# Optimization experiments

Measured on AMD Instinct MI355X. Metric: run time of the kernel, lower is better.

Reference implementation:

```python
import jax, jax.numpy as jnp
import numpy as np

B, T, D, H, F = 4, 2048, 512, 8, 2048
WINDOW = 128
HD = D // H
EPS = 1e-5


def layer_norm(x, g, b):
    mu = jnp.mean(x, axis=-1, keepdims=True)
    var = jnp.mean(jnp.square(x - mu), axis=-1, keepdims=True)
    return (x - mu) * jax.lax.rsqrt(var + EPS) * g + b


def setup_inputs() -> dict:
    key = jax.random.key(0)
    ks = jax.random.split(key, 5)
    s = 0.02
    return {
        "x": jax.random.normal(ks[0], (B, T, D), dtype=jnp.float32),
        "in_proj_w": jax.random.normal(ks[1], (3 * D, D), dtype=jnp.float32) * s,
        "in_proj_b": jnp.zeros((3 * D,), dtype=jnp.float32),
        "out_w": jax.random.normal(ks[2], (D, D), dtype=jnp.float32) * s,
        "out_b": jnp.zeros((D,), dtype=jnp.float32),
        "ln1_g": jnp.ones((D,), dtype=jnp.float32),
        "ln1_b": jnp.zeros((D,), dtype=jnp.float32),
        "ln2_g": jnp.ones((D,), dtype=jnp.float32),
        "ln2_b": jnp.zeros((D,), dtype=jnp.float32),
        "w1": jax.random.normal(ks[3], (F, D), dtype=jnp.float32) * s,
        "b1": jnp.zeros((F,), dtype=jnp.float32),
        "w2": jax.random.normal(ks[4], (D, F), dtype=jnp.float32) * s,
        "b2": jnp.zeros((D,), dtype=jnp.float32),
    }


def reference(x, in_proj_w, in_proj_b, out_w, out_b, ln1_g, ln1_b, ln2_g, ln2_b, w1, b1, w2, b2):
    # pre-norm sliding-window causal self-attention
    x2 = layer_norm(x, ln1_g, ln1_b)
    qkv = x2 @ in_proj_w.T + in_proj_b  # (B,T,3D)
    q, k, v = jnp.split(qkv, 3, axis=-1)
    q = q.reshape(B, T, H, HD)
    k = k.reshape(B, T, H, HD)
    v = v.reshape(B, T, H, HD)
    scale = 1.0 / np.sqrt(HD).astype(np.float32)
    scores = jnp.einsum("bthd,bshd->bhts", q, k) * scale  # dense (B,H,T,T)
    idx = jnp.arange(T)
    i = idx[:, None]
    j = idx[None, :]
    allowed = (j <= i) & (j >= i - WINDOW + 1)  # (T,T) bool, True = attend
    scores = jnp.where(allowed[None, None], scores, -jnp.inf)
    attn = jax.nn.softmax(scores, axis=-1)
    ctx = jnp.einsum("bhts,bshd->bthd", attn, v).reshape(B, T, D)
    attn_out = ctx @ out_w.T + out_b
    x = x + attn_out  # dropout is identity in eval
    # FFN block
    x3 = layer_norm(x, ln2_g, ln2_b)
    h = jax.nn.gelu(x3 @ w1.T + b1, approximate=False)
    x = x + h @ w2.T + b2
    return x
```

## Files before the change

### kernel.cpp

```cpp
#include <hip/hip_runtime.h>
#include <math.h>

constexpr int Bn = 4;
constexpr int Tn = 2048;
constexpr int Dn = 512;
constexpr int Hn = 8;
constexpr int HDn = 64;
constexpr int Fn = 2048;
constexpr int WIN = 128;
constexpr float EPS = 1e-5f;
constexpr int Mrows = Bn * Tn;
constexpr int QKVD = 3 * Dn;

using short8 = __attribute__((ext_vector_type(8))) short;
using f32x4  = __attribute__((ext_vector_type(4))) float;

__device__ __forceinline__ short f2bf(float f) {
    unsigned u = __float_as_uint(f);
    unsigned r = (u + 0x7FFFu + ((u >> 16) & 1u)) >> 16;
    return (short)r;
}

__device__ __forceinline__ float gelu_exact(float v) {
    return 0.5f * v * (1.0f + erff(v * 0.70710678118654752f));
}

__device__ __forceinline__ void async16(const short* g, short* l) {
    __builtin_amdgcn_global_load_lds(
        (const __attribute__((address_space(1))) void*)g,
        (__attribute__((address_space(3))) void*)l,
        16, 0, 0);
}

__global__ __launch_bounds__(256) void cvt_bf16(const float* __restrict__ src,
                                                short* __restrict__ dst, int n4)
{
    int i = blockIdx.x * 256 + threadIdx.x;
    if (i < n4) {
        float4 v = ((const float4*)src)[i];
        short4 o;
        o.x = f2bf(v.x); o.y = f2bf(v.y); o.z = f2bf(v.z); o.w = f2bf(v.w);
        ((short4*)dst)[i] = o;
    }
}

__global__ __launch_bounds__(64) void ln_kernel(const float* __restrict__ x,
                                                const float* __restrict__ g,
                                                const float* __restrict__ b,
                                                short* __restrict__ y)
{
    int row = blockIdx.x;
    int lane = threadIdx.x;
    const float4* xr = (const float4*)(x + (size_t)row * Dn);
    float4 v0 = xr[lane];
    float4 v1 = xr[lane + 64];
    float s = v0.x + v0.y + v0.z + v0.w + v1.x + v1.y + v1.z + v1.w;
#pragma unroll
    for (int off = 32; off >= 1; off >>= 1) s += __shfl_xor(s, off, 64);
    float mu = s * (1.0f / Dn);
    float d0x = v0.x - mu, d0y = v0.y - mu, d0z = v0.z - mu, d0w = v0.w - mu;
    float d1x = v1.x - mu, d1y = v1.y - mu, d1z = v1.z - mu, d1w = v1.w - mu;
    float q = d0x*d0x + d0y*d0y + d0z*d0z + d0w*d0w
            + d1x*d1x + d1y*d1y + d1z*d1z + d1w*d1w;
#pragma unroll
    for (int off = 32; off >= 1; off >>= 1) q += __shfl_xor(q, off, 64);
    float inv = rsqrtf(q * (1.0f / Dn) + EPS);
    const float4* gr = (const float4*)g;
    const float4* br = (const float4*)b;
    float4 g0 = gr[lane], g1 = gr[lane + 64];
    float4 b0 = br[lane], b1 = br[lane + 64];
    short4 a0, a1;
    a0.x = f2bf(d0x * inv * g0.x + b0.x);
    a0.y = f2bf(d0y * inv * g0.y + b0.y);
    a0.z = f2bf(d0z * inv * g0.z + b0.z);
    a0.w = f2bf(d0w * inv * g0.w + b0.w);
    a1.x = f2bf(d1x * inv * g1.x + b1.x);
    a1.y = f2bf(d1y * inv * g1.y + b1.y);
    a1.z = f2bf(d1z * inv * g1.z + b1.z);
    a1.w = f2bf(d1w * inv * g1.w + b1.w);
    short4* yr = (short4*)(y + (size_t)row * Dn);
    yr[lane] = a0;
    yr[lane + 64] = a1;
}

template <int MODE, int BK>
__global__ __launch_bounds__(256) void gemm_mfma(const short* __restrict__ A,
                                                 const short* __restrict__ Bw,
                                                 const float* __restrict__ bias,
                                                 const float* __restrict__ resid,
                                                 void* __restrict__ Cout,
                                                 short* __restrict__ q_out,
                                                 short* __restrict__ k_out,
                                                 short* __restrict__ v_out,
                                                 int M, int N, int K)
{
    constexpr int NCH = BK / 8;
    constexpr int LGN = (BK == 32) ? 2 : 3;
    constexpr int RPI = 512 / BK;
    constexpr int NI  = 32 / RPI;
    constexpr int BUF = 128 * BK;
    constexpr int KK  = BK / 32;
    constexpr int SMSZ = (4 * BUF > 17408) ? 4 * BUF : 17408;
    __shared__ short SMEM[SMSZ];
    short* Asb = SMEM;
    short* Bsb = SMEM + 2 * BUF;

    int tid = threadIdx.x;
    int w = tid >> 6, lane = tid & 63;
    int wr = w >> 1, wc = w & 1;
    int m0 = blockIdx.y * 128, n0 = blockIdx.x * 128;
    int quad = lane >> 4, l16 = lane & 15;

    f32x4 zero = {0.f, 0.f, 0.f, 0.f};
    f32x4 acc[4][4];
#pragma unroll
    for (int i = 0; i < 4; ++i)
#pragma unroll
        for (int j = 0; j < 4; ++j) acc[i][j] = zero;

    int rl = lane >> LGN;
    int ch = lane & (NCH - 1);
    const short* Ag[NI];
    const short* Bg[NI];
    int ldsOff[NI];
#pragma unroll
    for (int s = 0; s < NI; ++s) {
        int rowl = w * 32 + s * RPI + rl;
        int csw = (ch ^ ((rowl * BK >> 6) & (NCH - 1))) * 8;
        Ag[s] = A + (size_t)(m0 + rowl) * K + csw;
        Bg[s] = Bw + (size_t)(n0 + rowl) * K + csw;
        ldsOff[s] = (w * 32 + s * RPI) * BK;
    }

    auto stage = [&](int kt, int pp) {
#pragma unroll
        for (int s = 0; s < NI; ++s) {
            async16(Ag[s] + kt, Asb + pp * BUF + ldsOff[s]);
            async16(Bg[s] + kt, Bsb + pp * BUF + ldsOff[s]);
        }
    };

    stage(0, 0);
    int p = 0;
    for (int kt = 0; kt < K; kt += BK) {
        __syncthreads();
        if (kt + BK < K) stage(kt + BK, p ^ 1);
        short8 aF[KK][4], bF[KK][4];
#pragma unroll
        for (int kk = 0; kk < KK; ++kk)
#pragma unroll
            for (int i = 0; i < 4; ++i) {
                int ra = wr * 64 + i * 16 + l16;
                int rb = wc * 64 + i * 16 + l16;
                int cs = ((kk * 4 + quad) ^ ((ra * BK >> 6) & (NCH - 1))) * 8;
                aF[kk][i] = *(const short8*)(Asb + p * BUF + ra * BK + cs);
                bF[kk][i] = *(const short8*)(Bsb + p * BUF + rb * BK + cs);
            }
#pragma unroll
        for (int kk = 0; kk < KK; ++kk)
#pragma unroll
            for (int i = 0; i < 4; ++i)
#pragma unroll
                for (int j = 0; j < 4; ++j)
                    acc[i][j] = __builtin_amdgcn_mfma_f32_16x16x32_bf16(
                        aF[kk][i], bF[kk][j], acc[i][j], 0, 0, 0);
        p ^= 1;
    }

    if constexpr (MODE == 3) {
        __syncthreads();
        short* rp = SMEM + w * 4352;
        int b = m0 >> 11;
        int ncol0 = n0 + wc * 64;
        int sec = ncol0 >> 9;
        int h = (ncol0 & 511) >> 6;
        int bh = b * 8 + h;
        int t0 = (m0 & 2047) + wr * 64;
        if (sec == 2) {
#pragma unroll
            for (int j = 0; j < 4; ++j) {
                int d = j * 16 + l16;
                float bv = bias[ncol0 + j * 16 + l16];
#pragma unroll
                for (int i = 0; i < 4; ++i)
#pragma unroll
                    for (int r = 0; r < 4; ++r)
                        rp[d * 68 + i * 16 + quad * 4 + r] = f2bf(acc[i][j][r] + bv);
            }
#pragma unroll
            for (int it = 0; it < 8; ++it) {
                int row = it * 8 + (lane >> 3);
                int off = (lane & 7) * 8;
                *(short8*)(v_out + ((size_t)bh * 64 + row) * 2048 + t0 + off) =
                    *(const short8*)(rp + row * 68 + off);
            }
        } else {
            short* dst = (sec == 0 ? q_out : k_out);
#pragma unroll
            for (int j = 0; j < 4; ++j) {
                int d = j * 16 + l16;
                float bv = bias[ncol0 + j * 16 + l16];
#pragma unroll
                for (int i = 0; i < 4; ++i)
#pragma unroll
                    for (int r = 0; r < 4; ++r)
                        rp[(i * 16 + quad * 4 + r) * 68 + d] = f2bf(acc[i][j][r] + bv);
            }
#pragma unroll
            for (int it = 0; it < 8; ++it) {
                int row = it * 8 + (lane >> 3);
                int off = (lane & 7) * 8;
                *(short8*)(dst + ((size_t)bh * 2048 + t0 + row) * 64 + off) =
                    *(const short8*)(rp + row * 68 + off);
            }
        }
        return;
    }

    if constexpr (MODE == 2) {
        __syncthreads();
        short* rp = SMEM + w * 4352;
        short* Cb = (short*)Cout;
#pragma unroll
        for (int j = 0; j < 4; ++j) {
            float bv = bias[n0 + wc * 64 + j * 16 + l16];
#pragma unroll
            for (int i = 0; i < 4; ++i)
#pragma unroll
                for (int r = 0; r < 4; ++r)
                    rp[(i * 16 + quad * 4 + r) * 68 + j * 16 + l16] =
                        f2bf(gelu_exact(acc[i][j][r] + bv));
        }
#pragma unroll
        for (int it = 0; it < 8; ++it) {
            int row = it * 8 + (lane >> 3);
            int off = (lane & 7) * 8;
            *(short8*)(Cb + (size_t)(m0 + wr * 64 + row) * N + n0 + wc * 64 + off) =
                *(const short8*)(rp + row * 68 + off);
        }
        return;
    }

    float* Cf = (float*)Cout;
#pragma unroll
    for (int j = 0; j < 4; ++j) {
        int n = n0 + wc * 64 + j * 16 + l16;
        float bv = bias[n];
#pragma unroll
        for (int i = 0; i < 4; ++i) {
            int mbase = m0 + wr * 64 + i * 16 + quad * 4;
#pragma unroll
            for (int r = 0; r < 4; ++r) {
                size_t idx = (size_t)(mbase + r) * N + n;
                Cf[idx] = acc[i][j][r] + bv + resid[idx];
            }
        }
    }
}

constexpr int QS = 72;
constexpr int VS = 200;

__global__ __launch_bounds__(256) void attn_mfma(const short* __restrict__ Qg,
                                                 const short* __restrict__ Kg,
                                                 const short* __restrict__ Vtg,
                                                 short* __restrict__ ctx)
{
    __shared__ short Qs[64 * QS];
    __shared__ short Ks[192 * QS];
    __shared__ short Vt[64 * VS];
    int tid = threadIdx.x;
    int w = tid >> 6, lane = tid & 63, quad = lane >> 4, l16 = lane & 15;
    int blk = blockIdx.x;
    int q0 = (blk & 31) << 6;
    int bh = blk >> 5;
    int kbase = q0 - 128;

    {
        const short* src = Qg + ((size_t)bh * 2048 + q0) * 64;
        for (int c = tid; c < 512; c += 256) {
            int row = c >> 3, off = (c & 7) * 8;
            *(short8*)(Qs + row * QS + off) = *(const short8*)(src + row * 64 + off);
        }
    }
    {
        const short* base = Kg + (size_t)bh * 2048 * 64;
        for (int c = tid; c < 1536; c += 256) {
            int row = c >> 3, off = (c & 7) * 8;
            int srow = kbase + row; srow = srow < 0 ? 0 : srow;
            *(short8*)(Ks + row * QS + off) = *(const short8*)(base + (size_t)srow * 64 + off);
        }
    }
    {
        const short* base = Vtg + (size_t)bh * 64 * 2048;
        for (int c = tid; c < 1536; c += 256) {
            int row = c / 24, cc = c - row * 24;
            int off = cc * 8;
            int scol = kbase + off; scol = scol < 0 ? 0 : scol;
            *(short8*)(Vt + row * VS + off) = *(const short8*)(base + (size_t)row * 2048 + scol);
        }
    }
    __syncthreads();

    short8 aF0 = *(const short8*)(Qs + (w * 16 + l16) * QS + quad * 8);
    short8 aF1 = *(const short8*)(Qs + (w * 16 + l16) * QS + 32 + quad * 8);
    f32x4 S[12];
    f32x4 zero = {0.f, 0.f, 0.f, 0.f};
#pragma unroll
    for (int t = 0; t < 12; ++t) S[t] = zero;
#pragma unroll
    for (int t = 0; t < 12; ++t) {
        short8 b0 = *(const short8*)(Ks + (t * 16 + l16) * QS + quad * 8);
        short8 b1 = *(const short8*)(Ks + (t * 16 + l16) * QS + 32 + quad * 8);
        S[t] = __builtin_amdgcn_mfma_f32_16x16x32_bf16(aF0, b0, S[t], 0, 0, 0);
        S[t] = __builtin_amdgcn_mfma_f32_16x16x32_bf16(aF1, b1, S[t], 0, 0, 0);
    }

    int i0 = w * 16 + quad * 4;
    float mrow[4] = {-INFINITY, -INFINITY, -INFINITY, -INFINITY};
#pragma unroll
    for (int t = 0; t < 12; ++t) {
        int jl = t * 16 + l16;
        int kg = kbase + jl;
#pragma unroll
        for (int r = 0; r < 4; ++r) {
            int dj = jl - (i0 + r);
            bool ok = (dj >= 1) && (dj <= 128) && (kg >= 0);
            float s = ok ? S[t][r] * 0.125f : -INFINITY;
            S[t][r] = s;
            mrow[r] = fmaxf(mrow[r], s);
        }
    }
#pragma unroll
    for (int off = 8; off >= 1; off >>= 1)
#pragma unroll
        for (int r = 0; r < 4; ++r)
            mrow[r] = fmaxf(mrow[r], __shfl_xor(mrow[r], off, 64));
    float sum[4] = {0.f, 0.f, 0.f, 0.f};
#pragma unroll
    for (int t = 0; t < 12; ++t)
#pragma unroll
        for (int r = 0; r < 4; ++r) {
            float p = __expf(S[t][r] - mrow[r]);
            S[t][r] = p;
            sum[r] += p;
        }
#pragma unroll
    for (int off = 8; off >= 1; off >>= 1)
#pragma unroll
        for (int r = 0; r < 4; ++r)
            sum[r] += __shfl_xor(sum[r], off, 64);
    float inv[4];
#pragma unroll
    for (int r = 0; r < 4; ++r) inv[r] = 1.0f / sum[r];

    __syncthreads();
    short* Ps = Ks;
#pragma unroll
    for (int t = 0; t < 12; ++t)
#pragma unroll
        for (int r = 0; r < 4; ++r)
            Ps[(w * 16 + quad * 4 + r) * VS + t * 16 + l16] = f2bf(S[t][r]);

    f32x4 O[4];
#pragma unroll
    for (int tN = 0; tN < 4; ++tN) O[tN] = zero;
#pragma unroll
    for (int s = 0; s < 6; ++s) {
        short8 aP = *(const short8*)(Ps + (w * 16 + l16) * VS + s * 32 + quad * 8);
#pragma unroll
        for (int tN = 0; tN < 4; ++tN) {
            short8 bV = *(const short8*)(Vt + (tN * 16 + l16) * VS + s * 32 + quad * 8);
            O[tN] = __builtin_amdgcn_mfma_f32_16x16x32_bf16(aP, bV, O[tN], 0, 0, 0);
        }
    }

    int b = bh >> 3, h = bh & 7;
#pragma unroll
    for (int tN = 0; tN < 4; ++tN)
#pragma unroll
        for (int r = 0; r < 4; ++r) {
            int trow = q0 + w * 16 + quad * 4 + r;
            ctx[((size_t)(b * 2048 + trow)) * 512 + h * 64 + tN * 16 + l16] =
                f2bf(O[tN][r] * inv[r]);
        }
}

extern "C" void kernel_launch(void* const* d_in, const int* in_sizes, int n_in,
                              void* d_out, int out_size, void* d_ws, size_t ws_size,
                              hipStream_t stream)
{
    const float* x         = (const float*)d_in[0];
    const float* in_proj_w = (const float*)d_in[1];
    const float* in_proj_b = (const float*)d_in[2];
    const float* out_w     = (const float*)d_in[3];
    const float* out_b     = (const float*)d_in[4];
    const float* ln1_g     = (const float*)d_in[5];
    const float* ln1_b     = (const float*)d_in[6];
    const float* ln2_g     = (const float*)d_in[7];
    const float* ln2_b     = (const float*)d_in[8];
    const float* w1        = (const float*)d_in[9];
    const float* b1        = (const float*)d_in[10];
    const float* w2        = (const float*)d_in[11];
    const float* b2        = (const float*)d_in[12];
    float* out = (float*)d_out;

    char* ws = (char*)d_ws;
    short* attnQ = (short*)ws;
    short* attnK = (short*)(ws + (size_t)8 * 1024 * 1024);
    short* attnV = (short*)(ws + (size_t)16 * 1024 * 1024);
    short* hbuf  = (short*)ws;
    short* regB  = (short*)(ws + (size_t)32 * 1024 * 1024);
    short* wq  = (short*)(ws + (size_t)40 * 1024 * 1024);
    short* wo  = wq + (size_t)QKVD * Dn;
    short* w1b = wo + (size_t)Dn * Dn;
    short* w2b = w1b + (size_t)Fn * Dn;

    cvt_bf16<<<(QKVD * Dn / 4 + 255) / 256, 256, 0, stream>>>(in_proj_w, wq, QKVD * Dn / 4);
    cvt_bf16<<<(Dn * Dn / 4 + 255) / 256, 256, 0, stream>>>(out_w, wo, Dn * Dn / 4);
    cvt_bf16<<<(Fn * Dn / 4 + 255) / 256, 256, 0, stream>>>(w1, w1b, Fn * Dn / 4);
    cvt_bf16<<<(Dn * Fn / 4 + 255) / 256, 256, 0, stream>>>(w2, w2b, Dn * Fn / 4);

    ln_kernel<<<Mrows, 64, 0, stream>>>(x, ln1_g, ln1_b, regB);
    gemm_mfma<3, 32><<<dim3(QKVD / 128, Mrows / 128), 256, 0, stream>>>(
        regB, wq, in_proj_b, nullptr, nullptr, attnQ, attnK, attnV, Mrows, QKVD, Dn);
    attn_mfma<<<Bn * Hn * (Tn / 64), 256, 0, stream>>>(attnQ, attnK, attnV, regB);
    gemm_mfma<1, 64><<<dim3(Dn / 128, Mrows / 128), 256, 0, stream>>>(
        regB, wo, out_b, x, out, nullptr, nullptr, nullptr, Mrows, Dn, Dn);
    ln_kernel<<<Mrows, 64, 0, stream>>>(out, ln2_g, ln2_b, regB);
    gemm_mfma<2, 32><<<dim3(Fn / 128, Mrows / 128), 256, 0, stream>>>(
        regB, w1b, b1, nullptr, hbuf, nullptr, nullptr, nullptr, Mrows, Fn, Dn);
    gemm_mfma<1, 64><<<dim3(Dn / 128, Mrows / 128), 256, 0, stream>>>(
        hbuf, w2b, b2, out, out, nullptr, nullptr, nullptr, Mrows, Dn, Fn);
}
```

Baseline: 234.5 us.

## Remap GEMM blocks for XCD locality, shrink epilogue LDS, fuse weight casts

The GEMM grid becomes 1D and block ids are remapped so that each XCD (bid & 7) works on its own set of M tiles and iterates across N. The aim is better L2 reuse of A tiles within a chiplet. The staged epilogues for the QKV and GELU modes now write out in two 32-row phases, so the LDS array can drop the 17408-short floor and use only 4*BUF, which may raise occupancy for the BK=32 kernels. The four weight-conversion launches are merged into one kernel with hardcoded range boundaries, which trims launch overhead but ties that kernel to these exact shapes.

```diff
diff --git a/kernel.cpp b/kernel.cpp
--- a/kernel.cpp
+++ b/kernel.cpp
@@ -32,16 +32,25 @@
         16, 0, 0);
 }
 
-__global__ __launch_bounds__(256) void cvt_bf16(const float* __restrict__ src,
-                                                short* __restrict__ dst, int n4)
+__global__ __launch_bounds__(256) void cvt_all(const float* __restrict__ s0,
+                                               const float* __restrict__ s1,
+                                               const float* __restrict__ s2,
+                                               const float* __restrict__ s3,
+                                               short* __restrict__ d0,
+                                               short* __restrict__ d1,
+                                               short* __restrict__ d2,
+                                               short* __restrict__ d3)
 {
     int i = blockIdx.x * 256 + threadIdx.x;
-    if (i < n4) {
-        float4 v = ((const float4*)src)[i];
-        short4 o;
-        o.x = f2bf(v.x); o.y = f2bf(v.y); o.z = f2bf(v.z); o.w = f2bf(v.w);
-        ((short4*)dst)[i] = o;
-    }
+    const float* src; short* dst; int j;
+    if (i < 196608)      { src = s0; dst = d0; j = i; }
+    else if (i < 262144) { src = s1; dst = d1; j = i - 196608; }
+    else if (i < 524288) { src = s2; dst = d2; j = i - 262144; }
+    else                 { src = s3; dst = d3; j = i - 524288; }
+    float4 v = ((const float4*)src)[j];
+    short4 o;
+    o.x = f2bf(v.x); o.y = f2bf(v.y); o.z = f2bf(v.z); o.w = f2bf(v.w);
+    ((short4*)dst)[j] = o;
 }
 
 __global__ __launch_bounds__(64) void ln_kernel(const float* __restrict__ x,
@@ -100,15 +109,19 @@
     constexpr int NI  = 32 / RPI;
     constexpr int BUF = 128 * BK;
     constexpr int KK  = BK / 32;
-    constexpr int SMSZ = (4 * BUF > 17408) ? 4 * BUF : 17408;
-    __shared__ short SMEM[SMSZ];
+    __shared__ short SMEM[4 * BUF];
     short* Asb = SMEM;
     short* Bsb = SMEM + 2 * BUF;
 
     int tid = threadIdx.x;
     int w = tid >> 6, lane = tid & 63;
     int wr = w >> 1, wc = w & 1;
-    int m0 = blockIdx.y * 128, n0 = blockIdx.x * 128;
+    int nN = N >> 7;
+    int bid = blockIdx.x;
+    int xcd = bid & 7, sq = bid >> 3;
+    int mi = xcd + 8 * (sq / nN);
+    int ni = sq % nN;
+    int m0 = mi * 128, n0 = ni * 128;
     int quad = lane >> 4, l16 = lane & 15;
 
     f32x4 zero = {0.f, 0.f, 0.f, 0.f};
@@ -169,7 +182,7 @@
 
     if constexpr (MODE == 3) {
         __syncthreads();
-        short* rp = SMEM + w * 4352;
+        short* rp = SMEM + w * 2176;
         int b = m0 >> 11;
         int ncol0 = n0 + wc * 64;
         int sec = ncol0 >> 9;
@@ -178,65 +191,78 @@
         int t0 = (m0 & 2047) + wr * 64;
         if (sec == 2) {
 #pragma unroll
-            for (int j = 0; j < 4; ++j) {
-                int d = j * 16 + l16;
-                float bv = bias[ncol0 + j * 16 + l16];
-#pragma unroll
-                for (int i = 0; i < 4; ++i)
+            for (int ph = 0; ph < 2; ++ph) {
+#pragma unroll
+                for (int j = 2 * ph; j < 2 * ph + 2; ++j) {
+                    int dl = (j - 2 * ph) * 16 + l16;
+                    float bv = bias[ncol0 + j * 16 + l16];
+#pragma unroll
+                    for (int i = 0; i < 4; ++i)
+#pragma unroll
+                        for (int r = 0; r < 4; ++r)
+                            rp[dl * 68 + i * 16 + quad * 4 + r] = f2bf(acc[i][j][r] + bv);
+                }
+#pragma unroll
+                for (int it = 0; it < 4; ++it) {
+                    int row = it * 8 + (lane >> 3);
+                    int off = (lane & 7) * 8;
+                    *(short8*)(v_out + ((size_t)bh * 64 + 32 * ph + row) * 2048 + t0 + off) =
+                        *(const short8*)(rp + row * 68 + off);
+                }
+            }
+        } else {
+            short* dst = (sec == 0 ? q_out : k_out);
+#pragma unroll
+            for (int ph = 0; ph < 2; ++ph) {
+#pragma unroll
+                for (int i = 2 * ph; i < 2 * ph + 2; ++i) {
+                    int tl = (i - 2 * ph) * 16 + quad * 4;
+#pragma unroll
+                    for (int j = 0; j < 4; ++j) {
+                        float bv = bias[ncol0 + j * 16 + l16];
+#pragma unroll
+                        for (int r = 0; r < 4; ++r)
+                            rp[(tl + r) * 68 + j * 16 + l16] = f2bf(acc[i][j][r] + bv);
+                    }
+                }
+#pragma unroll
+                for (int it = 0; it < 4; ++it) {
+                    int row = it * 8 + (lane >> 3);
+                    int off = (lane & 7) * 8;
+                    *(short8*)(dst + ((size_t)bh * 2048 + t0 + 32 * ph + row) * 64 + off) =
+                        *(const short8*)(rp + row * 68 + off);
+                }
+            }
+        }
+        return;
+    }
+
+    if constexpr (MODE == 2) {
+        __syncthreads();
+        short* rp = SMEM + w * 2176;
+        short* Cb = (short*)Cout;
+#pragma unroll
+        for (int ph = 0; ph < 2; ++ph) {
+#pragma unroll
+            for (int i = 2 * ph; i < 2 * ph + 2; ++i) {
+                int ml = (i - 2 * ph) * 16 + quad * 4;
+#pragma unroll
+                for (int j = 0; j < 4; ++j) {
+                    float bv = bias[n0 + wc * 64 + j * 16 + l16];
 #pragma unroll
                     for (int r = 0; r < 4; ++r)
-                        rp[d * 68 + i * 16 + quad * 4 + r] = f2bf(acc[i][j][r] + bv);
-            }
-#pragma unroll
-            for (int it = 0; it < 8; ++it) {
+                        rp[(ml + r) * 68 + j * 16 + l16] =
+                            f2bf(gelu_exact(acc[i][j][r] + bv));
+                }
+            }
+#pragma unroll
+            for (int it = 0; it < 4; ++it) {
                 int row = it * 8 + (lane >> 3);
                 int off = (lane & 7) * 8;
-                *(short8*)(v_out + ((size_t)bh * 64 + row) * 2048 + t0 + off) =
+                *(short8*)(Cb + (size_t)(m0 + wr * 64 + 32 * ph + row) * N
+                              + n0 + wc * 64 + off) =
                     *(const short8*)(rp + row * 68 + off);
             }
-        } else {
-            short* dst = (sec == 0 ? q_out : k_out);
-#pragma unroll
-            for (int j = 0; j < 4; ++j) {
-                int d = j * 16 + l16;
-                float bv = bias[ncol0 + j * 16 + l16];
-#pragma unroll
-                for (int i = 0; i < 4; ++i)
-#pragma unroll
-                    for (int r = 0; r < 4; ++r)
-                        rp[(i * 16 + quad * 4 + r) * 68 + d] = f2bf(acc[i][j][r] + bv);
-            }
-#pragma unroll
-            for (int it = 0; it < 8; ++it) {
-                int row = it * 8 + (lane >> 3);
-                int off = (lane & 7) * 8;
-                *(short8*)(dst + ((size_t)bh * 2048 + t0 + row) * 64 + off) =
-                    *(const short8*)(rp + row * 68 + off);
-            }
-        }
-        return;
-    }
-
-    if constexpr (MODE == 2) {
-        __syncthreads();
-        short* rp = SMEM + w * 4352;
-        short* Cb = (short*)Cout;
-#pragma unroll
-        for (int j = 0; j < 4; ++j) {
-            float bv = bias[n0 + wc * 64 + j * 16 + l16];
-#pragma unroll
-            for (int i = 0; i < 4; ++i)
-#pragma unroll
-                for (int r = 0; r < 4; ++r)
-                    rp[(i * 16 + quad * 4 + r) * 68 + j * 16 + l16] =
-                        f2bf(gelu_exact(acc[i][j][r] + bv));
-        }
-#pragma unroll
-        for (int it = 0; it < 8; ++it) {
-            int row = it * 8 + (lane >> 3);
-            int off = (lane & 7) * 8;
-            *(short8*)(Cb + (size_t)(m0 + wr * 64 + row) * N + n0 + wc * 64 + off) =
-                *(const short8*)(rp + row * 68 + off);
         }
         return;
     }
@@ -416,20 +442,17 @@
     short* w1b = wo + (size_t)Dn * Dn;
     short* w2b = w1b + (size_t)Fn * Dn;
 
-    cvt_bf16<<<(QKVD * Dn / 4 + 255) / 256, 256, 0, stream>>>(in_proj_w, wq, QKVD * Dn / 4);
-    cvt_bf16<<<(Dn * Dn / 4 + 255) / 256, 256, 0, stream>>>(out_w, wo, Dn * Dn / 4);
-    cvt_bf16<<<(Fn * Dn / 4 + 255) / 256, 256, 0, stream>>>(w1, w1b, Fn * Dn / 4);
-    cvt_bf16<<<(Dn * Fn / 4 + 255) / 256, 256, 0, stream>>>(w2, w2b, Dn * Fn / 4);
+    cvt_all<<<3072, 256, 0, stream>>>(in_proj_w, out_w, w1, w2, wq, wo, w1b, w2b);
 
     ln_kernel<<<Mrows, 64, 0, stream>>>(x, ln1_g, ln1_b, regB);
-    gemm_mfma<3, 32><<<dim3(QKVD / 128, Mrows / 128), 256, 0, stream>>>(
+    gemm_mfma<3, 32><<<(Mrows / 128) * (QKVD / 128), 256, 0, stream>>>(
         regB, wq, in_proj_b, nullptr, nullptr, attnQ, attnK, attnV, Mrows, QKVD, Dn);
     attn_mfma<<<Bn * Hn * (Tn / 64), 256, 0, stream>>>(attnQ, attnK, attnV, regB);
-    gemm_mfma<1, 64><<<dim3(Dn / 128, Mrows / 128), 256, 0, stream>>>(
+    gemm_mfma<1, 64><<<(Mrows / 128) * (Dn / 128), 256, 0, stream>>>(
         regB, wo, out_b, x, out, nullptr, nullptr, nullptr, Mrows, Dn, Dn);
     ln_kernel<<<Mrows, 64, 0, stream>>>(out, ln2_g, ln2_b, regB);
-    gemm_mfma<2, 32><<<dim3(Fn / 128, Mrows / 128), 256, 0, stream>>>(
+    gemm_mfma<2, 32><<<(Mrows / 128) * (Fn / 128), 256, 0, stream>>>(
         regB, w1b, b1, nullptr, hbuf, nullptr, nullptr, nullptr, Mrows, Fn, Dn);
-    gemm_mfma<1, 64><<<dim3(Dn / 128, Mrows / 128), 256, 0, stream>>>(
+    gemm_mfma<1, 64><<<(Mrows / 128) * (Dn / 128), 256, 0, stream>>>(
         hbuf, w2b, b2, out, out, nullptr, nullptr, nullptr, Mrows, Dn, Fn);
 }
```

New measurement: 223.3 us. 1.05x faster.
